# Optimization experiments

Hardware: AMD Instinct MI355X
Metric: run time of the kernel (lower is better)

## Reference

```python
import jax, jax.numpy as jnp
import numpy as np

NUM_HEAD = 8


def setup_inputs() -> dict:
    key = jax.random.key(0)
    k1, k2, k3, k4 = jax.random.split(key, 4)
    B, C, H, W = 16, 512, 64, 64
    x = jax.random.normal(k1, (B, C, H, W), dtype=jnp.float32)
    w_qkv = jax.random.normal(k2, (3 * C, C), dtype=jnp.float32) * 0.02  # Conv2d 1x1, no bias
    w_proj = jax.random.normal(k3, (C, C), dtype=jnp.float32) * 0.02
    b_proj = jax.random.normal(k4, (C,), dtype=jnp.float32) * 0.02
    return {"x": x, "w_qkv": w_qkv, "w_proj": w_proj, "b_proj": b_proj}


def reference(x, w_qkv, w_proj, b_proj):
    B, C, H, W = x.shape
    nh = NUM_HEAD
    hd = C // nh
    scale = hd ** (-0.5)
    # 1x1 conv == channel matmul
    qkv = jnp.einsum('oc,bchw->bohw', w_qkv, x)  # [B, 3C, H, W]
    q, k, v = jnp.split(qkv, 3, axis=1)
    q = q.reshape(B, nh, hd, H * W)
    k = k.reshape(B, nh, hd, H * W)
    v = v.reshape(B, nh, hd, H * W)
    # NOTE: faithful to source: contracts over the spatial (last) axis,
    # producing a [B, nh, hd, hd] matrix.
    attn = jnp.einsum('bnqd,bnkd->bnqk', q, k) * scale
    attn = jax.nn.softmax(attn, axis=-1)
    # Faithful to source: 'k' and 'v' are both summed independently (outer sum),
    # exactly as torch.einsum computes it.
    out = jnp.einsum('bnqk,bnvd->bnqd', attn, v)
    out = out.reshape(B, C, H, W)
    return jnp.einsum('oc,bchw->bohw', w_proj, out) + b_proj[None, :, None, None]
```

## Files before the change

### kernel.cpp

```cpp
#include <hip/hip_runtime.h>

#define CDIM 512
#define NH 8
#define HWDIM 4096
#define TILE 256

__global__ __launch_bounds__(256) void prep_kernel(
    const float* __restrict__ wqkv, const float* __restrict__ wproj,
    float* __restrict__ wvT, float* __restrict__ wp) {
  int idx = blockIdx.x * 256 + threadIdx.x;
  if (idx < 4096) {
    int c = idx >> 3, n = idx & 7;
    const float* p = wqkv + (size_t)(1024 + n * 64) * CDIM + c;
    float s = 0.f;
#pragma unroll 8
    for (int j = 0; j < 64; ++j) s += p[(size_t)j * CDIM];
    wvT[idx] = s;
  } else if (idx < 8192) {
    int i2 = idx - 4096;
    int o = i2 >> 3, n = i2 & 7;
    const float* p = wproj + (size_t)o * CDIM + n * 64;
    float s = 0.f;
#pragma unroll 8
    for (int j = 0; j < 64; ++j) s += p[j];
    wp[i2] = s;
  }
}

__global__ __launch_bounds__(256) void fused_kernel(
    const float* __restrict__ x, const float* __restrict__ bias,
    const float* __restrict__ wvT, const float* __restrict__ wp,
    float* __restrict__ y) {
  __shared__ __align__(16) float sWv[4096];
  __shared__ __align__(16) float sWp[4096];
  __shared__ __align__(16) float sB[512];
  __shared__ __align__(16) float sS[4][NH][TILE];

  const int t = threadIdx.x;
  for (int i = t; i < 4096; i += 256) { sWv[i] = wvT[i]; sWp[i] = wp[i]; }
  for (int i = t; i < 512; i += 256) sB[i] = bias[i];
  __syncthreads();

  const int wave = t >> 6;
  const int lane = t & 63;
  const int pos0 = blockIdx.x * TILE;
  const int b = pos0 >> 12;
  const int hw0 = pos0 & (HWDIM - 1);
  const float* xb = x + ((size_t)b * CDIM) * HWDIM + hw0 + lane * 4;

  float acc[NH][4];
#pragma unroll
  for (int n = 0; n < NH; ++n) {
    acc[n][0] = 0.f; acc[n][1] = 0.f; acc[n][2] = 0.f; acc[n][3] = 0.f;
  }

  const int c0 = wave * 128;
#pragma unroll 8
  for (int cc = 0; cc < 128; ++cc) {
    const int c = c0 + cc;
    const float4 xv = *(const float4*)(xb + (size_t)c * HWDIM);
    const float4 w0 = *(const float4*)&sWv[c * 8];
    const float4 w1 = *(const float4*)&sWv[c * 8 + 4];
    const float wn[8] = {w0.x, w0.y, w0.z, w0.w, w1.x, w1.y, w1.z, w1.w};
    const float xv4[4] = {xv.x, xv.y, xv.z, xv.w};
#pragma unroll
    for (int n = 0; n < NH; ++n) {
#pragma unroll
      for (int p = 0; p < 4; ++p) acc[n][p] = fmaf(wn[n], xv4[p], acc[n][p]);
    }
  }

#pragma unroll
  for (int n = 0; n < NH; ++n) {
    *(float4*)&sS[wave][n][lane * 4] =
        make_float4(acc[n][0], acc[n][1], acc[n][2], acc[n][3]);
  }
  __syncthreads();

  float S4[NH][4];
#pragma unroll
  for (int n = 0; n < NH; ++n) {
    const float4 a0 = *(const float4*)&sS[0][n][lane * 4];
    const float4 a1 = *(const float4*)&sS[1][n][lane * 4];
    const float4 a2 = *(const float4*)&sS[2][n][lane * 4];
    const float4 a3 = *(const float4*)&sS[3][n][lane * 4];
    S4[n][0] = a0.x + a1.x + a2.x + a3.x;
    S4[n][1] = a0.y + a1.y + a2.y + a3.y;
    S4[n][2] = a0.z + a1.z + a2.z + a3.z;
    S4[n][3] = a0.w + a1.w + a2.w + a3.w;
  }

  float* yb = y + ((size_t)b * CDIM) * HWDIM + hw0 + lane * 4;
  const int o0 = wave * 128;
#pragma unroll 4
  for (int oo = 0; oo < 128; ++oo) {
    const int o = o0 + oo;
    const float4 w0 = *(const float4*)&sWp[o * 8];
    const float4 w1 = *(const float4*)&sWp[o * 8 + 4];
    const float wn[8] = {w0.x, w0.y, w0.z, w0.w, w1.x, w1.y, w1.z, w1.w};
    const float bb = sB[o];
    float r[4] = {bb, bb, bb, bb};
#pragma unroll
    for (int n = 0; n < NH; ++n) {
#pragma unroll
      for (int p = 0; p < 4; ++p) r[p] = fmaf(wn[n], S4[n][p], r[p]);
    }
    *(float4*)(yb + (size_t)o * HWDIM) = make_float4(r[0], r[1], r[2], r[3]);
  }
}

extern "C" void kernel_launch(void* const* d_in, const int* in_sizes, int n_in,
                              void* d_out, int out_size, void* d_ws, size_t ws_size,
                              hipStream_t stream) {
  const float* x     = (const float*)d_in[0];
  const float* wqkv  = (const float*)d_in[1];
  const float* wproj = (const float*)d_in[2];
  const float* bproj = (const float*)d_in[3];
  float* y = (float*)d_out;

  float* wvT = (float*)d_ws;
  float* wp  = wvT + 4096;

  prep_kernel<<<32, 256, 0, stream>>>(wqkv, wproj, wvT, wp);
  fused_kernel<<<256, 256, 0, stream>>>(x, bproj, wvT, wp, y);
}
```

Measured before the change: 269.6 us.

## Split fused kernel into separate reduction and projection kernels for more blocks

Splits the single fused kernel into two. s_kernel reduces x into per-head sums S over 512 blocks, with 8 channel groups per block and 8 batched float4 loads per thread. y_kernel reads S from a workspace buffer and writes the output over 512 blocks, each handling 64 output channels. This targets the low occupancy of only 256 blocks on a large-CU GPU and puts more loads in flight. The cost is an extra launch and a round trip of the small S intermediate through global memory.

```diff
diff --git a/kernel.cpp b/kernel.cpp
--- a/kernel.cpp
+++ b/kernel.cpp
@@ -3,7 +3,6 @@
 #define CDIM 512
 #define NH 8
 #define HWDIM 4096
-#define TILE 256
 
 __global__ __launch_bounds__(256) void prep_kernel(
     const float* __restrict__ wqkv, const float* __restrict__ wproj,
@@ -27,73 +26,92 @@
   }
 }
 
-__global__ __launch_bounds__(256) void fused_kernel(
-    const float* __restrict__ x, const float* __restrict__ bias,
-    const float* __restrict__ wvT, const float* __restrict__ wp,
-    float* __restrict__ y) {
+__global__ __launch_bounds__(256) void s_kernel(
+    const float* __restrict__ x, const float* __restrict__ wvT,
+    float* __restrict__ S) {
   __shared__ __align__(16) float sWv[4096];
-  __shared__ __align__(16) float sWp[4096];
-  __shared__ __align__(16) float sB[512];
-  __shared__ __align__(16) float sS[4][NH][TILE];
+  __shared__ __align__(16) float sPart[NH][8][32][4];
 
   const int t = threadIdx.x;
-  for (int i = t; i < 4096; i += 256) { sWv[i] = wvT[i]; sWp[i] = wp[i]; }
-  for (int i = t; i < 512; i += 256) sB[i] = bias[i];
+  for (int i = t; i < 4096; i += 256) sWv[i] = wvT[i];
   __syncthreads();
 
-  const int wave = t >> 6;
-  const int lane = t & 63;
-  const int pos0 = blockIdx.x * TILE;
-  const int b = pos0 >> 12;
-  const int hw0 = pos0 & (HWDIM - 1);
-  const float* xb = x + ((size_t)b * CDIM) * HWDIM + hw0 + lane * 4;
+  const int cg = t >> 5;
+  const int slot = t & 31;
+  const int wb = blockIdx.x;
+  const int b = wb >> 5;
+  const int hw0 = (wb & 31) * 128;
+  const float* xb = x + ((size_t)b * CDIM) * HWDIM + hw0 + slot * 4;
 
   float acc[NH][4];
 #pragma unroll
-  for (int n = 0; n < NH; ++n) {
-    acc[n][0] = 0.f; acc[n][1] = 0.f; acc[n][2] = 0.f; acc[n][3] = 0.f;
-  }
+  for (int n = 0; n < NH; ++n) { acc[n][0] = acc[n][1] = acc[n][2] = acc[n][3] = 0.f; }
 
-  const int c0 = wave * 128;
-#pragma unroll 8
-  for (int cc = 0; cc < 128; ++cc) {
-    const int c = c0 + cc;
-    const float4 xv = *(const float4*)(xb + (size_t)c * HWDIM);
-    const float4 w0 = *(const float4*)&sWv[c * 8];
-    const float4 w1 = *(const float4*)&sWv[c * 8 + 4];
-    const float wn[8] = {w0.x, w0.y, w0.z, w0.w, w1.x, w1.y, w1.z, w1.w};
-    const float xv4[4] = {xv.x, xv.y, xv.z, xv.w};
+  const int c0 = cg * 64;
+  for (int g = 0; g < 8; ++g) {
+    float4 xv[8];
 #pragma unroll
-    for (int n = 0; n < NH; ++n) {
+    for (int j = 0; j < 8; ++j)
+      xv[j] = *(const float4*)(xb + (size_t)(c0 + g * 8 + j) * HWDIM);
 #pragma unroll
-      for (int p = 0; p < 4; ++p) acc[n][p] = fmaf(wn[n], xv4[p], acc[n][p]);
+    for (int j = 0; j < 8; ++j) {
+      const int c = c0 + g * 8 + j;
+      const float4 w0 = *(const float4*)&sWv[c * 8];
+      const float4 w1 = *(const float4*)&sWv[c * 8 + 4];
+      const float wn[8] = {w0.x, w0.y, w0.z, w0.w, w1.x, w1.y, w1.z, w1.w};
+      const float xr[4] = {xv[j].x, xv[j].y, xv[j].z, xv[j].w};
+#pragma unroll
+      for (int n = 0; n < NH; ++n) {
+#pragma unroll
+        for (int p = 0; p < 4; ++p) acc[n][p] = fmaf(wn[n], xr[p], acc[n][p]);
+      }
     }
   }
 
 #pragma unroll
-  for (int n = 0; n < NH; ++n) {
-    *(float4*)&sS[wave][n][lane * 4] =
-        make_float4(acc[n][0], acc[n][1], acc[n][2], acc[n][3]);
-  }
+  for (int n = 0; n < NH; ++n)
+    *(float4*)&sPart[n][cg][slot][0] = make_float4(acc[n][0], acc[n][1], acc[n][2], acc[n][3]);
   __syncthreads();
 
-  float S4[NH][4];
+  const int n2 = t >> 5;
+  const int slot2 = t & 31;
+  float4 sum = make_float4(0.f, 0.f, 0.f, 0.f);
+#pragma unroll
+  for (int g = 0; g < 8; ++g) {
+    const float4 a = *(const float4*)&sPart[n2][g][slot2][0];
+    sum.x += a.x; sum.y += a.y; sum.z += a.z; sum.w += a.w;
+  }
+  *(float4*)&S[((size_t)b * NH + n2) * HWDIM + hw0 + slot2 * 4] = sum;
+}
+
+__global__ __launch_bounds__(256) void y_kernel(
+    const float* __restrict__ S, const float* __restrict__ wp,
+    const float* __restrict__ bias, float* __restrict__ y) {
+  __shared__ __align__(16) float sWp[4096];
+  __shared__ __align__(16) float sB[512];
+
+  const int t = threadIdx.x;
+  for (int i = t; i < 4096; i += 256) sWp[i] = wp[i];
+  for (int i = t; i < 512; i += 256) sB[i] = bias[i];
+  __syncthreads();
+
+  const int wb = blockIdx.x;
+  const int b = wb >> 5;
+  const int span = (wb >> 3) & 3;
+  const int og = wb & 7;
+  const int hwo = span * 1024 + t * 4;
+
+  float s[NH][4];
 #pragma unroll
   for (int n = 0; n < NH; ++n) {
-    const float4 a0 = *(const float4*)&sS[0][n][lane * 4];
-    const float4 a1 = *(const float4*)&sS[1][n][lane * 4];
-    const float4 a2 = *(const float4*)&sS[2][n][lane * 4];
-    const float4 a3 = *(const float4*)&sS[3][n][lane * 4];
-    S4[n][0] = a0.x + a1.x + a2.x + a3.x;
-    S4[n][1] = a0.y + a1.y + a2.y + a3.y;
-    S4[n][2] = a0.z + a1.z + a2.z + a3.z;
-    S4[n][3] = a0.w + a1.w + a2.w + a3.w;
+    const float4 a = *(const float4*)&S[((size_t)b * NH + n) * HWDIM + hwo];
+    s[n][0] = a.x; s[n][1] = a.y; s[n][2] = a.z; s[n][3] = a.w;
   }
 
-  float* yb = y + ((size_t)b * CDIM) * HWDIM + hw0 + lane * 4;
-  const int o0 = wave * 128;
+  float* yb = y + ((size_t)b * CDIM) * HWDIM + hwo;
+  const int o0 = og * 64;
 #pragma unroll 4
-  for (int oo = 0; oo < 128; ++oo) {
+  for (int oo = 0; oo < 64; ++oo) {
     const int o = o0 + oo;
     const float4 w0 = *(const float4*)&sWp[o * 8];
     const float4 w1 = *(const float4*)&sWp[o * 8 + 4];
@@ -103,7 +121,7 @@
 #pragma unroll
     for (int n = 0; n < NH; ++n) {
 #pragma unroll
-      for (int p = 0; p < 4; ++p) r[p] = fmaf(wn[n], S4[n][p], r[p]);
+      for (int p = 0; p < 4; ++p) r[p] = fmaf(wn[n], s[n][p], r[p]);
     }
     *(float4*)(yb + (size_t)o * HWDIM) = make_float4(r[0], r[1], r[2], r[3]);
   }
@@ -120,7 +138,9 @@
 
   float* wvT = (float*)d_ws;
   float* wp  = wvT + 4096;
+  float* S   = wp  + 4096;
 
   prep_kernel<<<32, 256, 0, stream>>>(wqkv, wproj, wvT, wp);
-  fused_kernel<<<256, 256, 0, stream>>>(x, bproj, wvT, wp, y);
+  s_kernel<<<512, 256, 0, stream>>>(x, wvT, S);
+  y_kernel<<<512, 256, 0, stream>>>(S, wp, bproj, y);
 }
```

Result: slower. 277.3 us (+2.9%).
